# Kernel tuning notes

Hardware: AMD Instinct MI355X
Metric: run time of the kernel (lower is better)

## Reference

```python
import jax, jax.numpy as jnp
import numpy as np
from jax import lax

HIDDEN = 256
WIDTH = 1024
DEPTH = 4
T = 64
SUBSTEPS = 8  # fixed RK4 substeps per save interval (replaces diffrax adaptive Tsit5)

Y0 = np.array([0.0008417, 0.01495894, 0.00082556, 0.00068982, 0.00063456,
               0.00832867, 0.00190631, 0.00155624, 0.00142264, 0.01858621,
               0.02000239, 0.01796071, 0.01670121, 0.22218046, 0.02531468,
               0.03337227, 0.6147068], dtype=np.float32)


def setup_inputs() -> dict:
    key = jax.random.key(0)
    ks = jax.random.split(key, 8)

    def lin(k, out, inp):
        kw, kb = jax.random.split(k)
        lim = 1.0 / np.sqrt(inp)
        W = jax.random.uniform(kw, (out, inp), jnp.float32, -lim, lim)
        b = jax.random.uniform(kb, (out,), jnp.float32, -lim, lim)
        return W, b

    W0, b0 = lin(ks[0], WIDTH, HIDDEN + 17)
    Whs, bhs = [], []
    for i in range(DEPTH - 1):
        w, b = lin(ks[1 + i], WIDTH, WIDTH)
        Whs.append(w)
        bhs.append(b)
    Wh = jnp.stack(Whs)   # [DEPTH-1, WIDTH, WIDTH]
    bh = jnp.stack(bhs)   # [DEPTH-1, WIDTH]
    Wl, bl = lin(ks[4], HIDDEN, WIDTH)
    beta_W, beta_b = lin(ks[5], 1, HIDDEN)
    hvec = 0.01 * jax.random.normal(ks[6], (HIDDEN,), jnp.float32)
    scale = jnp.array([0.1], jnp.float32)
    y0_log = jnp.log(jnp.asarray(Y0))
    ts = jnp.arange(T, dtype=jnp.float32) * 0.25  # save points (months)
    return dict(ts=ts, W0=W0, b0=b0, Wh=Wh, bh=bh, Wl=Wl, bl=bl,
                beta_W=beta_W, beta_b=beta_b, hvec=hvec, scale=scale,
                y0_log=y0_log)


def _forward(ts, W0, b0, Wh, bh, Wl, bl, beta_W, beta_b, hvec, scale, y0_log):
    xi, mu, sigma, nu, gamma = 13/12, 0.041/12, 91/12, 36/12, 1.8/12

    def mlp(x):  # softplus hidden activations, final tanh(0.01*x)
        z = jax.nn.softplus(W0 @ x + b0)
        def body(z, wb):
            w, b = wb
            return jax.nn.softplus(w @ z + b), None
        z, _ = lax.scan(body, z, (Wh, bh))
        return jnp.tanh(0.01 * (Wl @ z + bl))

    def rhs(y):  # y = concat(state[17], h[HIDDEN])
        state, h = y[:17], y[17:]
        bb1 = 8.0 * jax.nn.sigmoid(beta_W @ h + beta_b)[0] + 25.0
        bb2, bb3, bb4 = 0.5 * bb1, 0.35 * bb1, 0.25 * bb1
        M, S1, E1, E2, E3, E4, I1, I2, I3, I4, R1, R2, R3, R4, S2, S3, S4 = state
        I = I1 + I2 + I3 + I4
        R = R1 + R2 + R3 + R4
        dstate = jnp.stack([
            R * mu - (xi + mu) * M,
            mu * (1 - R) + xi * M - mu * S1 - bb1 * I * S1,
            bb1 * I * S1 - (mu + sigma) * E1,
            bb2 * I * S2 - (mu + sigma) * E2,
            bb3 * I * S3 - (mu + sigma) * E3,
            bb4 * I * S4 - (mu + sigma) * E4,
            sigma * E1 - (nu + mu) * I1,
            sigma * E2 - (nu + mu) * I2,
            sigma * E3 - (nu + mu) * I3,
            sigma * E4 - (nu + mu) * I4,
            nu * I1 - (mu + gamma) * R1,
            nu * I2 - (mu + gamma) * R2,
            nu * I3 - (mu + gamma) * R3,
            nu * I4 - (mu + gamma) * R4,
            gamma * R1 - mu * S2 - bb2 * I * S2,
            gamma * R2 - mu * S3 - bb3 * I * S3,
            gamma * (R3 + R4) - mu * S4 - bb4 * I * S4,
        ])
        dh = scale[0] * mlp(jnp.concatenate([h, state]))
        return jnp.concatenate([dstate, dh])

    def rk4(y, dt):
        k1 = rhs(y)
        k2 = rhs(y + 0.5 * dt * k1)
        k3 = rhs(y + 0.5 * dt * k2)
        k4 = rhs(y + dt * k3)
        return y + (dt / 6.0) * (k1 + 2 * k2 + 2 * k3 + k4)

    y0 = jnp.concatenate([jax.nn.softmax(y0_log), hvec])

    def interval(y, dt_i):
        dt = dt_i / SUBSTEPS
        def step(y, _):
            return rk4(y, dt), None
        y, _ = lax.scan(step, y, None, length=SUBSTEPS)
        return y, y

    dts = ts[1:] - ts[:-1]
    _, ys = lax.scan(interval, y0, dts)
    ys = jnp.concatenate([y0[None], ys], axis=0)  # [T, 17+HIDDEN]
    return ys[:, :17], ys[:, 17:]


def reference(ts, W0, b0, Wh, bh, Wl, bl, beta_W, beta_b, hvec, scale, y0_log):
    return _forward(ts, W0, b0, Wh, bh, Wl, bl, beta_W, beta_b, hvec, scale, y0_log)
```

## Files before the change

### kernel.cpp

```cpp
#include <hip/hip_runtime.h>
#include <math.h>

#define NBLK    32
#define NLAUNCH 256
#define BS      512
#define NSTATE  17
#define NH      256
#define NX      273
#define WID     1024
#define NT      64
#define NSUB    8
#define SLC     32
#define POLL_CAP 2000000

#define SCALE_P 32768.0f
#define INV_P   3.0517578125e-5f
#define BIAS_P  (1LL << 22)
#define BIAS32  (32LL << 22)
#define SCALE_D 1048576.0f
#define INV_D   9.5367431640625e-7f

typedef unsigned long long u64;
typedef unsigned int u32;

__device__ __forceinline__ float softplus_f(float v) {
    return fmaxf(v, 0.f) + log1pf(expf(-fabsf(v)));
}

__device__ __forceinline__ void acc_pack(u64* p, float p0, float p1) {
    long long q0 = llrintf(p0 * SCALE_P) + BIAS_P;
    long long q1 = llrintf(p1 * SCALE_P) + BIAS_P;
    u64 w = 1ULL + ((u64)q0 << 8) + ((u64)q1 << 36);
    asm volatile("global_atomic_add_x2 %0, %1, off" :: "v"(p), "v"(w) : "memory");
}
__device__ __forceinline__ void acc_dh(u64* p, float v) {
    long long q = llrintf(v * SCALE_D);
    u64 w = ((u64)q << 16) + 1ULL;
    asm volatile("global_atomic_add_x2 %0, %1, off" :: "v"(p), "v"(w) : "memory");
}
__device__ __forceinline__ u64 rmw_read(const u64* p) {
    u64 w;
    asm volatile("global_atomic_add_x2 %0, %1, %2, off sc0\n\t"
                 "s_waitcnt vmcnt(0)"
                 : "=&v"(w) : "v"(p), "v"(0ULL) : "memory");
    return w;
}
__device__ __forceinline__ void reset_async(u64* p) {
    asm volatile("global_atomic_swap_x2 %0, %1, off" :: "v"(p), "v"(0ULL) : "memory");
}

extern "C" __global__ __launch_bounds__(BS, 1) void ode_kernel(
    const float* __restrict__ ts,   const float* __restrict__ W0,
    const float* __restrict__ b0,   const float* __restrict__ Wh,
    const float* __restrict__ bh,   const float* __restrict__ Wl,
    const float* __restrict__ bl,   const float* __restrict__ betaW,
    const float* __restrict__ betab,const float* __restrict__ hvec,
    const float* __restrict__ scale,const float* __restrict__ y0log,
    float* __restrict__ out, u64* hacc1, u64* hacc2, u64* hacc3,
    u64* dhacc, unsigned* ctrl)
{
    const int t = threadIdx.x;

    __shared__ int role_sh;
    __shared__ __align__(16) float y_s[NX];
    __shared__ __align__(16) float yn_s[NX];
    __shared__ __align__(16) float xm[NX];
    __shared__ __align__(16) float k_s[NX];
    __shared__ __align__(16) float z1_s[SLC];
    __shared__ __align__(16) float h1_s[SLC];
    __shared__ __align__(16) float h2_s[SLC];
    __shared__ __align__(16) float h3_s[SLC];
    __shared__ float red[8];
    __shared__ float dt_sh;
    extern __shared__ float wh3c[];

    if (t == 0) {
        int xcd;
        asm volatile("s_getreg_b32 %0, hwreg(HW_REG_XCC_ID)" : "=s"(xcd));
        xcd &= 7;
        unsigned rk = atomicAdd(&ctrl[xcd], 1u);
        if (rk == NBLK - 1) atomicCAS(&ctrl[8], 0u, (unsigned)(xcd + 1));
        unsigned w; int it = 0;
        do {
            w = __hip_atomic_load(&ctrl[8], __ATOMIC_RELAXED, __HIP_MEMORY_SCOPE_AGENT);
        } while (w == 0u && ++it < POLL_CAP);
        role_sh = (w != 0u && xcd == (int)w - 1 && rk < NBLK) ? (int)rk : -1;
    }
    __syncthreads();
    const int blk = role_sh;
    if (blk < 0) return;

    const float scale0 = scale[0];
    const float betab0 = betab[0];

    const int rowH = t >> 4, laneH = t & 15;
    const int growH = blk * SLC + rowH;
    const int r0 = 2 * t, r1 = 2 * t + 1;

    const float b0r    = b0[growH];
    const float betaWr = (t < NH) ? betaW[t] : 0.f;
    const float blr    = (t < NH) ? bl[t] : 0.f;
    float bhc[3];
    float bhc_o[3];
    if (t < 16) {
        bhc[0]   = bh[blk * SLC + 2 * t];
        bhc_o[0] = bh[blk * SLC + 2 * t + 1];
        bhc[1]   = bh[WID + blk * SLC + 2 * t];
        bhc_o[1] = bh[WID + blk * SLC + 2 * t + 1];
        bhc[2]   = bh[2 * WID + blk * SLC + 2 * t];
        bhc_o[2] = bh[2 * WID + blk * SLC + 2 * t + 1];
    }

    float w0r[18];
    {
        const float* w0p = W0 + (size_t)growH * NX;
        #pragma unroll
        for (int i = 0; i < 18; i++) {
            int c = laneH + i * 16;
            w0r[i] = (c < NX) ? w0p[c] : 0.f;
        }
    }
    float4 wc1a[8], wc1b[8], wc2a[8], wc2b[8];
    {
        const float* base0 = Wh + (size_t)r0 * WID + blk * SLC;
        const float* base1 = Wh + (size_t)r1 * WID + blk * SLC;
        #pragma unroll
        for (int q = 0; q < 8; q++) {
            wc1a[q] = *(const float4*)(base0 + q * 4);
            wc1b[q] = *(const float4*)(base1 + q * 4);
            wc2a[q] = *(const float4*)(base0 + (size_t)WID * WID + q * 4);
            wc2b[q] = *(const float4*)(base1 + (size_t)WID * WID + q * 4);
        }
    }
    {
        const float* src = Wh + 2 * (size_t)WID * WID;
        for (int i = t; i < WID * 8; i += BS) {
            int r = i >> 3, q = i & 7;
            float4 v = *(const float4*)(src + (size_t)r * WID + blk * SLC + q * 4);
            wh3c[(q * 4 + 0) * WID + r] = v.x;
            wh3c[(q * 4 + 1) * WID + r] = v.y;
            wh3c[(q * 4 + 2) * WID + r] = v.z;
            wh3c[(q * 4 + 3) * WID + r] = v.w;
        }
    }

    if (t < NSTATE) {
        float m = -1e30f;
        for (int j = 0; j < NSTATE; j++) m = fmaxf(m, y0log[j]);
        float ssum = 0.f;
        for (int j = 0; j < NSTATE; j++) ssum += expf(y0log[j] - m);
        y_s[t] = expf(y0log[t] - m) / ssum;
    }
    if (t < NH) y_s[NSTATE + t] = hvec[t];
    __syncthreads();

    if (blk == 0) {
        if (t < NSTATE) out[t] = y_s[t];
        if (t < NH)     out[NT * NSTATE + t] = y_s[NSTATE + t];
    }

    const float c_xi = 13.f / 12.f, c_mu = 0.041f / 12.f, c_sig = 91.f / 12.f,
                c_nu = 36.f / 12.f, c_gam = 1.8f / 12.f;

    long long prev_dh = 0;
    unsigned sidx = 0;

    for (int iv = 0; iv < NT - 1; iv++) {
        if (t == 0) dt_sh = (ts[iv + 1] - ts[iv]) * (1.f / NSUB);
        __syncthreads();
        const float dt = dt_sh;

        for (int sub = 0; sub < NSUB; sub++) {
            if (t < NX) yn_s[t] = y_s[t];

            for (int s = 0; s < 4; s++) {
                const float a   = (s == 0) ? 0.f : ((s == 3) ? 1.f : 0.5f);
                const float wgt = ((s == 0) || (s == 3)) ? dt * (1.f / 6.f) : dt * (1.f / 3.f);
                const float adt = a * dt;
                ++sidx;
                const int par = (int)(sidx & 1u);
                u64* h1p = hacc1 + par * 512;
                u64* h2p = hacc2 + par * 512;
                u64* h3p = hacc3 + par * 512;

                if (t < NX) {
                    const int src = (t < NH) ? (NSTATE + t) : (t - NH);
                    float v = y_s[src];
                    if (s != 0) v = fmaf(adt, k_s[src], v);
                    xm[t] = v;
                }
                __syncthreads();

                {
                    float acc = 0.f;
                    #pragma unroll
                    for (int i = 0; i < 18; i++) {
                        int c = laneH + i * 16;
                        if (c < NX) acc = fmaf(w0r[i], xm[c], acc);
                    }
                    #pragma unroll
                    for (int m = 1; m < 16; m <<= 1) acc += __shfl_xor(acc, m, 16);
                    if (laneH == 0) z1_s[rowH] = softplus_f(acc + b0r);
                }
                if (t < NH) {
                    float p = betaWr * xm[t];
                    #pragma unroll
                    for (int m = 1; m < 64; m <<= 1) p += __shfl_xor(p, m, 64);
                    if ((t & 63) == 0) red[t >> 6] = p;
                }
                __syncthreads();

                {
                    float p0 = 0.f, p1 = 0.f;
                    #pragma unroll
                    for (int q = 0; q < 8; q++) {
                        float4 z = *(const float4*)(z1_s + q * 4);
                        p0 = fmaf(wc1a[q].x, z.x, p0); p0 = fmaf(wc1a[q].y, z.y, p0);
                        p0 = fmaf(wc1a[q].z, z.z, p0); p0 = fmaf(wc1a[q].w, z.w, p0);
                        p1 = fmaf(wc1b[q].x, z.x, p1); p1 = fmaf(wc1b[q].y, z.y, p1);
                        p1 = fmaf(wc1b[q].z, z.z, p1); p1 = fmaf(wc1b[q].w, z.w, p1);
                    }
                    acc_pack(h1p + t, p0, p1);
                }

                if (t == 256) {
                    const float* xs = xm + NH;
                    float sd  = red[0] + red[1] + red[2] + red[3] + betab0;
                    float bb1 = 8.f / (1.f + expf(-sd)) + 25.f;
                    float bb2 = 0.5f * bb1, bb3 = 0.35f * bb1, bb4 = 0.25f * bb1;
                    float M  = xs[0],  S1 = xs[1],  E1 = xs[2],  E2 = xs[3];
                    float E3 = xs[4],  E4 = xs[5],  I1 = xs[6],  I2 = xs[7];
                    float I3 = xs[8],  I4 = xs[9],  R1 = xs[10], R2 = xs[11];
                    float R3 = xs[12], R4 = xs[13], S2 = xs[14], S3 = xs[15];
                    float S4 = xs[16];
                    float I = I1 + I2 + I3 + I4, Rs = R1 + R2 + R3 + R4;
                    k_s[0]  = Rs * c_mu - (c_xi + c_mu) * M;
                    k_s[1]  = c_mu * (1.f - Rs) + c_xi * M - c_mu * S1 - bb1 * I * S1;
                    k_s[2]  = bb1 * I * S1 - (c_mu + c_sig) * E1;
                    k_s[3]  = bb2 * I * S2 - (c_mu + c_sig) * E2;
                    k_s[4]  = bb3 * I * S3 - (c_mu + c_sig) * E3;
                    k_s[5]  = bb4 * I * S4 - (c_mu + c_sig) * E4;
                    k_s[6]  = c_sig * E1 - (c_nu + c_mu) * I1;
                    k_s[7]  = c_sig * E2 - (c_nu + c_mu) * I2;
                    k_s[8]  = c_sig * E3 - (c_nu + c_mu) * I3;
                    k_s[9]  = c_sig * E4 - (c_nu + c_mu) * I4;
                    k_s[10] = c_nu * I1 - (c_mu + c_gam) * R1;
                    k_s[11] = c_nu * I2 - (c_mu + c_gam) * R2;
                    k_s[12] = c_nu * I3 - (c_mu + c_gam) * R3;
                    k_s[13] = c_nu * I4 - (c_mu + c_gam) * R4;
                    k_s[14] = c_gam * R1 - c_mu * S2 - bb2 * I * S2;
                    k_s[15] = c_gam * R2 - c_mu * S3 - bb3 * I * S3;
                    k_s[16] = c_gam * (R3 + R4) - c_mu * S4 - bb4 * I * S4;
                }

                if (t < 16) {
                    u64* p = h1p + blk * 16 + t;
                    u64 w; int it = 0;
                    do { w = rmw_read(p); } while ((w & 0xFFu) != 32u && ++it < POLL_CAP);
                    reset_async(p);
                    long long v0 = (long long)((w >> 8) & 0xFFFFFFFULL) - BIAS32;
                    long long v1 = (long long)(w >> 36) - BIAS32;
                    h1_s[2 * t]     = softplus_f((float)v0 * INV_P + bhc[0]);
                    h1_s[2 * t + 1] = softplus_f((float)v1 * INV_P + bhc_o[0]);
                }
                __syncthreads();

                {
                    float p0 = 0.f, p1 = 0.f;
                    #pragma unroll
                    for (int q = 0; q < 8; q++) {
                        float4 z = *(const float4*)(h1_s + q * 4);
                        p0 = fmaf(wc2a[q].x, z.x, p0); p0 = fmaf(wc2a[q].y, z.y, p0);
                        p0 = fmaf(wc2a[q].z, z.z, p0); p0 = fmaf(wc2a[q].w, z.w, p0);
                        p1 = fmaf(wc2b[q].x, z.x, p1); p1 = fmaf(wc2b[q].y, z.y, p1);
                        p1 = fmaf(wc2b[q].z, z.z, p1); p1 = fmaf(wc2b[q].w, z.w, p1);
                    }
                    acc_pack(h2p + t, p0, p1);
                }
                if (t < 16) {
                    u64* p = h2p + blk * 16 + t;
                    u64 w; int it = 0;
                    do { w = rmw_read(p); } while ((w & 0xFFu) != 32u && ++it < POLL_CAP);
                    reset_async(p);
                    long long v0 = (long long)((w >> 8) & 0xFFFFFFFULL) - BIAS32;
                    long long v1 = (long long)(w >> 36) - BIAS32;
                    h2_s[2 * t]     = softplus_f((float)v0 * INV_P + bhc[1]);
                    h2_s[2 * t + 1] = softplus_f((float)v1 * INV_P + bhc_o[1]);
                }
                __syncthreads();

                {
                    float p0 = 0.f, p1 = 0.f;
                    #pragma unroll
                    for (int j = 0; j < SLC; j++) {
                        float hv = h2_s[j];
                        float2 wv = *(const float2*)(wh3c + j * WID + r0);
                        p0 = fmaf(wv.x, hv, p0);
                        p1 = fmaf(wv.y, hv, p1);
                    }
                    acc_pack(h3p + t, p0, p1);
                }
                float4 wvL[8];
                if (t < NH) {
                    const float* wp = Wl + (size_t)t * WID + blk * SLC;
                    #pragma unroll
                    for (int q = 0; q < 8; q++) wvL[q] = *(const float4*)(wp + q * 4);
                }
                if (t < 16) {
                    u64* p = h3p + blk * 16 + t;
                    u64 w; int it = 0;
                    do { w = rmw_read(p); } while ((w & 0xFFu) != 32u && ++it < POLL_CAP);
                    reset_async(p);
                    long long v0 = (long long)((w >> 8) & 0xFFFFFFFULL) - BIAS32;
                    long long v1 = (long long)(w >> 36) - BIAS32;
                    h3_s[2 * t]     = softplus_f((float)v0 * INV_P + bhc[2]);
                    h3_s[2 * t + 1] = softplus_f((float)v1 * INV_P + bhc_o[2]);
                }
                __syncthreads();

                if (t < NH) {
                    float p = 0.f;
                    #pragma unroll
                    for (int q = 0; q < 8; q++) {
                        float4 z = *(const float4*)(h3_s + q * 4);
                        p = fmaf(wvL[q].x, z.x, p); p = fmaf(wvL[q].y, z.y, p);
                        p = fmaf(wvL[q].z, z.z, p); p = fmaf(wvL[q].w, z.w, p);
                    }
                    acc_dh(dhacc + t, p);

                    u64* dp = dhacc + t;
                    const u32 tgt = (32u * sidx) & 0xFFFFu;
                    u64 w; int it = 0;
                    do { w = rmw_read(dp); } while ((u32)(w & 0xFFFFu) != tgt && ++it < POLL_CAP);
                    long long val = ((long long)w) >> 16;
                    long long diff = val - prev_dh;
                    prev_dh = val;
                    float accv = (float)diff * INV_D;
                    k_s[NSTATE + t] = scale0 * tanhf(0.01f * (accv + blr));
                }
                __syncthreads();
                if (t < NX) yn_s[t] = fmaf(wgt, k_s[t], yn_s[t]);
            }

            __syncthreads();
            if (t < NX) y_s[t] = yn_s[t];
            __syncthreads();
        }

        if (blk == 0) {
            if (t < NSTATE) out[(iv + 1) * NSTATE + t] = y_s[t];
            if (t < NH)     out[NT * NSTATE + (iv + 1) * NH + t] = y_s[NSTATE + t];
        }
    }
}

extern "C" void kernel_launch(void* const* d_in, const int* in_sizes, int n_in,
                              void* d_out, int out_size, void* d_ws, size_t ws_size,
                              hipStream_t stream) {
    const float* ts    = (const float*)d_in[0];
    const float* W0    = (const float*)d_in[1];
    const float* b0    = (const float*)d_in[2];
    const float* Wh    = (const float*)d_in[3];
    const float* bh    = (const float*)d_in[4];
    const float* Wl    = (const float*)d_in[5];
    const float* bl    = (const float*)d_in[6];
    const float* betaW = (const float*)d_in[7];
    const float* betab = (const float*)d_in[8];
    const float* hvec  = (const float*)d_in[9];
    const float* scale = (const float*)d_in[10];
    const float* y0log = (const float*)d_in[11];
    float* out = (float*)d_out;

    u64*      hacc1 = (u64*)d_ws;
    u64*      hacc2 = (u64*)((char*)d_ws + 8192);
    u64*      hacc3 = (u64*)((char*)d_ws + 16384);
    u64*      dhacc = (u64*)((char*)d_ws + 24576);
    unsigned* ctrl  = (unsigned*)((char*)d_ws + 26624);

    static int lds_set = 0;
    if (!lds_set) {
        hipFuncSetAttribute((const void*)ode_kernel,
                            hipFuncAttributeMaxDynamicSharedMemorySize, 131072);
        lds_set = 1;
    }

    hipMemsetAsync(d_ws, 0, 26624 + 64, stream);
    hipLaunchKernelGGL(ode_kernel, dim3(NLAUNCH), dim3(BS), 131072, stream,
                       ts, W0, b0, Wh, bh, Wl, bl, betaW, betab, hvec, scale,
                       y0log, out, hacc1, hacc2, hacc3, dhacc, ctrl);
}
```

Before: 21.15 ms.

## Pack final-layer dh accumulation into paired atomics with parity buffers and sleep polling

The final Wl layer now has each of 128 threads compute two output rows and push both in one packed 64-bit atomic. This replaces the per-row running-sum dh accumulator with parity double-buffered counters that are reset asynchronously during the next stage, halving the atomic traffic and the number of polling threads on the final reduction. All spin waits move into a helper that inserts s_sleep between polls to reduce contention on the atomic lines. Risks are lower dh precision (SCALE_P instead of SCALE_D), added polling latency from the sleep, and reliance on the reset of the other parity buffer being ordered correctly.

```diff
diff --git a/kernel.cpp b/kernel.cpp
--- a/kernel.cpp
+++ b/kernel.cpp
@@ -11,14 +11,12 @@
 #define NT      64
 #define NSUB    8
 #define SLC     32
-#define POLL_CAP 2000000
+#define POLL_CAP 500000
 
 #define SCALE_P 32768.0f
 #define INV_P   3.0517578125e-5f
 #define BIAS_P  (1LL << 22)
 #define BIAS32  (32LL << 22)
-#define SCALE_D 1048576.0f
-#define INV_D   9.5367431640625e-7f
 
 typedef unsigned long long u64;
 typedef unsigned int u32;
@@ -31,11 +29,6 @@
     long long q0 = llrintf(p0 * SCALE_P) + BIAS_P;
     long long q1 = llrintf(p1 * SCALE_P) + BIAS_P;
     u64 w = 1ULL + ((u64)q0 << 8) + ((u64)q1 << 36);
-    asm volatile("global_atomic_add_x2 %0, %1, off" :: "v"(p), "v"(w) : "memory");
-}
-__device__ __forceinline__ void acc_dh(u64* p, float v) {
-    long long q = llrintf(v * SCALE_D);
-    u64 w = ((u64)q << 16) + 1ULL;
     asm volatile("global_atomic_add_x2 %0, %1, off" :: "v"(p), "v"(w) : "memory");
 }
 __device__ __forceinline__ u64 rmw_read(const u64* p) {
@@ -47,6 +40,15 @@
 }
 __device__ __forceinline__ void reset_async(u64* p) {
     asm volatile("global_atomic_swap_x2 %0, %1, off" :: "v"(p), "v"(0ULL) : "memory");
+}
+__device__ __forceinline__ u64 poll32(const u64* p) {
+    u64 w; int it = 0;
+    for (;;) {
+        w = rmw_read(p);
+        if ((w & 0xFFu) == 32u || ++it > POLL_CAP) break;
+        asm volatile("s_sleep 1");
+    }
+    return w;
 }
 
 extern "C" __global__ __launch_bounds__(BS, 1) void ode_kernel(
@@ -83,7 +85,7 @@
         unsigned w; int it = 0;
         do {
             w = __hip_atomic_load(&ctrl[8], __ATOMIC_RELAXED, __HIP_MEMORY_SCOPE_AGENT);
-        } while (w == 0u && ++it < POLL_CAP);
+        } while (w == 0u && ++it < 2000000);
         role_sh = (w != 0u && xcd == (int)w - 1 && rk < NBLK) ? (int)rk : -1;
     }
     __syncthreads();
@@ -99,9 +101,9 @@
 
     const float b0r    = b0[growH];
     const float betaWr = (t < NH) ? betaW[t] : 0.f;
-    const float blr    = (t < NH) ? bl[t] : 0.f;
-    float bhc[3];
-    float bhc_o[3];
+    float bl0 = 0.f, bl1 = 0.f;
+    if (t < 128) { bl0 = bl[2 * t]; bl1 = bl[2 * t + 1]; }
+    float bhc[3], bhc_o[3];
     if (t < 16) {
         bhc[0]   = bh[blk * SLC + 2 * t];
         bhc_o[0] = bh[blk * SLC + 2 * t + 1];
@@ -162,7 +164,6 @@
     const float c_xi = 13.f / 12.f, c_mu = 0.041f / 12.f, c_sig = 91.f / 12.f,
                 c_nu = 36.f / 12.f, c_gam = 1.8f / 12.f;
 
-    long long prev_dh = 0;
     unsigned sidx = 0;
 
     for (int iv = 0; iv < NT - 1; iv++) {
@@ -182,6 +183,8 @@
                 u64* h1p = hacc1 + par * 512;
                 u64* h2p = hacc2 + par * 512;
                 u64* h3p = hacc3 + par * 512;
+                u64* dhp = dhacc + par * 128;
+                u64* dhq = dhacc + (par ^ 1) * 128;
 
                 if (t < NX) {
                     const int src = (t < NH) ? (NSTATE + t) : (t - NH);
@@ -255,9 +258,9 @@
 
                 if (t < 16) {
                     u64* p = h1p + blk * 16 + t;
-                    u64 w; int it = 0;
-                    do { w = rmw_read(p); } while ((w & 0xFFu) != 32u && ++it < POLL_CAP);
+                    u64 w = poll32(p);
                     reset_async(p);
+                    if (t < 4) reset_async(dhq + blk * 4 + t);
                     long long v0 = (long long)((w >> 8) & 0xFFFFFFFULL) - BIAS32;
                     long long v1 = (long long)(w >> 36) - BIAS32;
                     h1_s[2 * t]     = softplus_f((float)v0 * INV_P + bhc[0]);
@@ -279,8 +282,7 @@
                 }
                 if (t < 16) {
                     u64* p = h2p + blk * 16 + t;
-                    u64 w; int it = 0;
-                    do { w = rmw_read(p); } while ((w & 0xFFu) != 32u && ++it < POLL_CAP);
+                    u64 w = poll32(p);
                     reset_async(p);
                     long long v0 = (long long)((w >> 8) & 0xFFFFFFFULL) - BIAS32;
                     long long v1 = (long long)(w >> 36) - BIAS32;
@@ -300,16 +302,19 @@
                     }
                     acc_pack(h3p + t, p0, p1);
                 }
-                float4 wvL[8];
-                if (t < NH) {
-                    const float* wp = Wl + (size_t)t * WID + blk * SLC;
-                    #pragma unroll
-                    for (int q = 0; q < 8; q++) wvL[q] = *(const float4*)(wp + q * 4);
+                float4 wvL0[8], wvL1[8];
+                if (t < 128) {
+                    const float* wp0 = Wl + (size_t)(2 * t) * WID + blk * SLC;
+                    const float* wp1 = Wl + (size_t)(2 * t + 1) * WID + blk * SLC;
+                    #pragma unroll
+                    for (int q = 0; q < 8; q++) {
+                        wvL0[q] = *(const float4*)(wp0 + q * 4);
+                        wvL1[q] = *(const float4*)(wp1 + q * 4);
+                    }
                 }
                 if (t < 16) {
                     u64* p = h3p + blk * 16 + t;
-                    u64 w; int it = 0;
-                    do { w = rmw_read(p); } while ((w & 0xFFu) != 32u && ++it < POLL_CAP);
+                    u64 w = poll32(p);
                     reset_async(p);
                     long long v0 = (long long)((w >> 8) & 0xFFFFFFFULL) - BIAS32;
                     long long v1 = (long long)(w >> 36) - BIAS32;
@@ -318,25 +323,24 @@
                 }
                 __syncthreads();
 
-                if (t < NH) {
-                    float p = 0.f;
+                if (t < 128) {
+                    float p0 = 0.f, p1 = 0.f;
                     #pragma unroll
                     for (int q = 0; q < 8; q++) {
                         float4 z = *(const float4*)(h3_s + q * 4);
-                        p = fmaf(wvL[q].x, z.x, p); p = fmaf(wvL[q].y, z.y, p);
-                        p = fmaf(wvL[q].z, z.z, p); p = fmaf(wvL[q].w, z.w, p);
-                    }
-                    acc_dh(dhacc + t, p);
-
-                    u64* dp = dhacc + t;
-                    const u32 tgt = (32u * sidx) & 0xFFFFu;
-                    u64 w; int it = 0;
-                    do { w = rmw_read(dp); } while ((u32)(w & 0xFFFFu) != tgt && ++it < POLL_CAP);
-                    long long val = ((long long)w) >> 16;
-                    long long diff = val - prev_dh;
-                    prev_dh = val;
-                    float accv = (float)diff * INV_D;
-                    k_s[NSTATE + t] = scale0 * tanhf(0.01f * (accv + blr));
+                        p0 = fmaf(wvL0[q].x, z.x, p0); p0 = fmaf(wvL0[q].y, z.y, p0);
+                        p0 = fmaf(wvL0[q].z, z.z, p0); p0 = fmaf(wvL0[q].w, z.w, p0);
+                        p1 = fmaf(wvL1[q].x, z.x, p1); p1 = fmaf(wvL1[q].y, z.y, p1);
+                        p1 = fmaf(wvL1[q].z, z.z, p1); p1 = fmaf(wvL1[q].w, z.w, p1);
+                    }
+                    acc_pack(dhp + t, p0, p1);
+
+                    u64 w = poll32(dhp + t);
+                    long long v0 = (long long)((w >> 8) & 0xFFFFFFFULL) - BIAS32;
+                    long long v1 = (long long)(w >> 36) - BIAS32;
+                    float a0 = (float)v0 * INV_P, a1 = (float)v1 * INV_P;
+                    k_s[NSTATE + 2 * t]     = scale0 * tanhf(0.01f * (a0 + bl0));
+                    k_s[NSTATE + 2 * t + 1] = scale0 * tanhf(0.01f * (a1 + bl1));
                 }
                 __syncthreads();
                 if (t < NX) yn_s[t] = fmaf(wgt, k_s[t], yn_s[t]);
```

Result: slower. 27.36 ms (+29.4%).

## Repartition MLP into 4x8 block tiling with groups of 8 per atomic accumulator

Applied to the files above, without the earlier changes.

Each of the 32 blocks now owns a 128-column slice and a 128-row chunk of the hidden layers instead of a 32-column slice. So each packed atomic accumulator waits on 8 contributors rather than 32, and accumulator resets move off the critical polling path. Weights are no longer kept resident in registers or LDS; they are reloaded from global memory (L2/cache) every substep. This trades fewer cross-block contributors per sync for repeated weight traffic and a serial 69-step W0 loop per thread.

```diff
diff --git a/kernel.cpp b/kernel.cpp
--- a/kernel.cpp
+++ b/kernel.cpp
@@ -10,13 +10,12 @@
 #define WID     1024
 #define NT      64
 #define NSUB    8
-#define SLC     32
-#define POLL_CAP 2000000
+#define POLL_CAP 500000
 
 #define SCALE_P 32768.0f
 #define INV_P   3.0517578125e-5f
 #define BIAS_P  (1LL << 22)
-#define BIAS32  (32LL << 22)
+#define BIAS8   (8LL << 22)
 #define SCALE_D 1048576.0f
 #define INV_D   9.5367431640625e-7f
 
@@ -47,6 +46,11 @@
 }
 __device__ __forceinline__ void reset_async(u64* p) {
     asm volatile("global_atomic_swap_x2 %0, %1, off" :: "v"(p), "v"(0ULL) : "memory");
+}
+__device__ __forceinline__ u64 poll_cnt8(const u64* p) {
+    u64 w; int it = 0;
+    do { w = rmw_read(p); } while ((w & 0xFFu) != 8u && ++it < POLL_CAP);
+    return w;
 }
 
 extern "C" __global__ __launch_bounds__(BS, 1) void ode_kernel(
@@ -66,13 +70,14 @@
     __shared__ __align__(16) float yn_s[NX];
     __shared__ __align__(16) float xm[NX];
     __shared__ __align__(16) float k_s[NX];
-    __shared__ __align__(16) float z1_s[SLC];
-    __shared__ __align__(16) float h1_s[SLC];
-    __shared__ __align__(16) float h2_s[SLC];
-    __shared__ __align__(16) float h3_s[SLC];
+    __shared__ __align__(16) float z1_s[128];
+    __shared__ __align__(16) float h1_s[128];
+    __shared__ __align__(16) float h2_s[128];
+    __shared__ __align__(16) float h3_s[128];
     __shared__ float red[8];
     __shared__ float dt_sh;
-    extern __shared__ float wh3c[];
+    extern __shared__ float lds_pad[];
+    (void)lds_pad;
 
     if (t == 0) {
         int xcd;
@@ -83,7 +88,7 @@
         unsigned w; int it = 0;
         do {
             w = __hip_atomic_load(&ctrl[8], __ATOMIC_RELAXED, __HIP_MEMORY_SCOPE_AGENT);
-        } while (w == 0u && ++it < POLL_CAP);
+        } while (w == 0u && ++it < 2000000);
         role_sh = (w != 0u && xcd == (int)w - 1 && rk < NBLK) ? (int)rk : -1;
     }
     __syncthreads();
@@ -93,56 +98,34 @@
     const float scale0 = scale[0];
     const float betab0 = betab[0];
 
-    const int rowH = t >> 4, laneH = t & 15;
-    const int growH = blk * SLC + rowH;
-    const int r0 = 2 * t, r1 = 2 * t + 1;
-
-    const float b0r    = b0[growH];
+    const int sb = blk >> 2;
+    const int qb = blk & 3;
+
+    const int zrl = t >> 2, zc4 = t & 3;
+    const float b0r = b0[128 * sb + zrl];
+    const float* w0p = W0 + (size_t)(128 * sb + zrl) * NX;
+
+    const int pw   = t >> 2;
+    const int widx = 128 * qb + pw;
+    const int r0g  = 2 * widx;
+    const int colg = 128 * sb + 32 * zc4;
+    const int coll = 32 * zc4;
+    const float* w1a = Wh + (size_t)r0g * WID + colg;
+    const float* w1b = Wh + (size_t)(r0g + 1) * WID + colg;
+    const float* w2a = w1a + (size_t)WID * WID;
+    const float* w2b = w1b + (size_t)WID * WID;
+    const float* w3a = w2a + (size_t)WID * WID;
+    const float* w3b = w2b + (size_t)WID * WID;
+
+    float be[3], bo[3];
+    if (t < 64) {
+        be[0] = bh[128 * sb + 2 * t];            bo[0] = bh[128 * sb + 2 * t + 1];
+        be[1] = bh[WID + 128 * sb + 2 * t];      bo[1] = bh[WID + 128 * sb + 2 * t + 1];
+        be[2] = bh[2 * WID + 128 * sb + 2 * t];  bo[2] = bh[2 * WID + 128 * sb + 2 * t + 1];
+    }
+    const float* wlp = Wl + (size_t)t * WID + 128 * sb + 32 * qb;
+    const float blr  = (t < NH) ? bl[t] : 0.f;
     const float betaWr = (t < NH) ? betaW[t] : 0.f;
-    const float blr    = (t < NH) ? bl[t] : 0.f;
-    float bhc[3];
-    float bhc_o[3];
-    if (t < 16) {
-        bhc[0]   = bh[blk * SLC + 2 * t];
-        bhc_o[0] = bh[blk * SLC + 2 * t + 1];
-        bhc[1]   = bh[WID + blk * SLC + 2 * t];
-        bhc_o[1] = bh[WID + blk * SLC + 2 * t + 1];
-        bhc[2]   = bh[2 * WID + blk * SLC + 2 * t];
-        bhc_o[2] = bh[2 * WID + blk * SLC + 2 * t + 1];
-    }
-
-    float w0r[18];
-    {
-        const float* w0p = W0 + (size_t)growH * NX;
-        #pragma unroll
-        for (int i = 0; i < 18; i++) {
-            int c = laneH + i * 16;
-            w0r[i] = (c < NX) ? w0p[c] : 0.f;
-        }
-    }
-    float4 wc1a[8], wc1b[8], wc2a[8], wc2b[8];
-    {
-        const float* base0 = Wh + (size_t)r0 * WID + blk * SLC;
-        const float* base1 = Wh + (size_t)r1 * WID + blk * SLC;
-        #pragma unroll
-        for (int q = 0; q < 8; q++) {
-            wc1a[q] = *(const float4*)(base0 + q * 4);
-            wc1b[q] = *(const float4*)(base1 + q * 4);
-            wc2a[q] = *(const float4*)(base0 + (size_t)WID * WID + q * 4);
-            wc2b[q] = *(const float4*)(base1 + (size_t)WID * WID + q * 4);
-        }
-    }
-    {
-        const float* src = Wh + 2 * (size_t)WID * WID;
-        for (int i = t; i < WID * 8; i += BS) {
-            int r = i >> 3, q = i & 7;
-            float4 v = *(const float4*)(src + (size_t)r * WID + blk * SLC + q * 4);
-            wh3c[(q * 4 + 0) * WID + r] = v.x;
-            wh3c[(q * 4 + 1) * WID + r] = v.y;
-            wh3c[(q * 4 + 2) * WID + r] = v.z;
-            wh3c[(q * 4 + 3) * WID + r] = v.w;
-        }
-    }
 
     if (t < NSTATE) {
         float m = -1e30f;
@@ -193,14 +176,13 @@
 
                 {
                     float acc = 0.f;
-                    #pragma unroll
-                    for (int i = 0; i < 18; i++) {
-                        int c = laneH + i * 16;
-                        if (c < NX) acc = fmaf(w0r[i], xm[c], acc);
-                    }
-                    #pragma unroll
-                    for (int m = 1; m < 16; m <<= 1) acc += __shfl_xor(acc, m, 16);
-                    if (laneH == 0) z1_s[rowH] = softplus_f(acc + b0r);
+                    for (int i = 0; i < 69; i++) {
+                        int c = zc4 + 4 * i;
+                        if (c < NX) acc = fmaf(w0p[c], xm[c], acc);
+                    }
+                    acc += __shfl_xor(acc, 1, 4);
+                    acc += __shfl_xor(acc, 2, 4);
+                    if (zc4 == 0) z1_s[zrl] = softplus_f(acc + b0r);
                 }
                 if (t < NH) {
                     float p = betaWr * xm[t];
@@ -214,13 +196,17 @@
                     float p0 = 0.f, p1 = 0.f;
                     #pragma unroll
                     for (int q = 0; q < 8; q++) {
-                        float4 z = *(const float4*)(z1_s + q * 4);
-                        p0 = fmaf(wc1a[q].x, z.x, p0); p0 = fmaf(wc1a[q].y, z.y, p0);
-                        p0 = fmaf(wc1a[q].z, z.z, p0); p0 = fmaf(wc1a[q].w, z.w, p0);
-                        p1 = fmaf(wc1b[q].x, z.x, p1); p1 = fmaf(wc1b[q].y, z.y, p1);
-                        p1 = fmaf(wc1b[q].z, z.z, p1); p1 = fmaf(wc1b[q].w, z.w, p1);
-                    }
-                    acc_pack(h1p + t, p0, p1);
+                        float4 wa = *(const float4*)(w1a + 4 * q);
+                        float4 wb = *(const float4*)(w1b + 4 * q);
+                        float4 z  = *(const float4*)(z1_s + coll + 4 * q);
+                        p0 = fmaf(wa.x, z.x, p0); p0 = fmaf(wa.y, z.y, p0);
+                        p0 = fmaf(wa.z, z.z, p0); p0 = fmaf(wa.w, z.w, p0);
+                        p1 = fmaf(wb.x, z.x, p1); p1 = fmaf(wb.y, z.y, p1);
+                        p1 = fmaf(wb.z, z.z, p1); p1 = fmaf(wb.w, z.w, p1);
+                    }
+                    p0 += __shfl_xor(p0, 1, 4); p0 += __shfl_xor(p0, 2, 4);
+                    p1 += __shfl_xor(p1, 1, 4); p1 += __shfl_xor(p1, 2, 4);
+                    if (zc4 == 0) acc_pack(h1p + widx, p0, p1);
                 }
 
                 if (t == 256) {
@@ -253,15 +239,12 @@
                     k_s[16] = c_gam * (R3 + R4) - c_mu * S4 - bb4 * I * S4;
                 }
 
-                if (t < 16) {
-                    u64* p = h1p + blk * 16 + t;
-                    u64 w; int it = 0;
-                    do { w = rmw_read(p); } while ((w & 0xFFu) != 32u && ++it < POLL_CAP);
-                    reset_async(p);
-                    long long v0 = (long long)((w >> 8) & 0xFFFFFFFULL) - BIAS32;
-                    long long v1 = (long long)(w >> 36) - BIAS32;
-                    h1_s[2 * t]     = softplus_f((float)v0 * INV_P + bhc[0]);
-                    h1_s[2 * t + 1] = softplus_f((float)v1 * INV_P + bhc_o[0]);
+                if (t < 64) {
+                    u64 w = poll_cnt8(h1p + 64 * sb + t);
+                    long long v0 = (long long)((w >> 8) & 0xFFFFFFFULL) - BIAS8;
+                    long long v1 = (long long)(w >> 36) - BIAS8;
+                    h1_s[2 * t]     = softplus_f((float)v0 * INV_P + be[0]);
+                    h1_s[2 * t + 1] = softplus_f((float)v1 * INV_P + bo[0]);
                 }
                 __syncthreads();
 
@@ -269,52 +252,49 @@
                     float p0 = 0.f, p1 = 0.f;
                     #pragma unroll
                     for (int q = 0; q < 8; q++) {
-                        float4 z = *(const float4*)(h1_s + q * 4);
-                        p0 = fmaf(wc2a[q].x, z.x, p0); p0 = fmaf(wc2a[q].y, z.y, p0);
-                        p0 = fmaf(wc2a[q].z, z.z, p0); p0 = fmaf(wc2a[q].w, z.w, p0);
-                        p1 = fmaf(wc2b[q].x, z.x, p1); p1 = fmaf(wc2b[q].y, z.y, p1);
-                        p1 = fmaf(wc2b[q].z, z.z, p1); p1 = fmaf(wc2b[q].w, z.w, p1);
-                    }
-                    acc_pack(h2p + t, p0, p1);
-                }
-                if (t < 16) {
-                    u64* p = h2p + blk * 16 + t;
-                    u64 w; int it = 0;
-                    do { w = rmw_read(p); } while ((w & 0xFFu) != 32u && ++it < POLL_CAP);
-                    reset_async(p);
-                    long long v0 = (long long)((w >> 8) & 0xFFFFFFFULL) - BIAS32;
-                    long long v1 = (long long)(w >> 36) - BIAS32;
-                    h2_s[2 * t]     = softplus_f((float)v0 * INV_P + bhc[1]);
-                    h2_s[2 * t + 1] = softplus_f((float)v1 * INV_P + bhc_o[1]);
+                        float4 wa = *(const float4*)(w2a + 4 * q);
+                        float4 wb = *(const float4*)(w2b + 4 * q);
+                        float4 z  = *(const float4*)(h1_s + coll + 4 * q);
+                        p0 = fmaf(wa.x, z.x, p0); p0 = fmaf(wa.y, z.y, p0);
+                        p0 = fmaf(wa.z, z.z, p0); p0 = fmaf(wa.w, z.w, p0);
+                        p1 = fmaf(wb.x, z.x, p1); p1 = fmaf(wb.y, z.y, p1);
+                        p1 = fmaf(wb.z, z.z, p1); p1 = fmaf(wb.w, z.w, p1);
+                    }
+                    p0 += __shfl_xor(p0, 1, 4); p0 += __shfl_xor(p0, 2, 4);
+                    p1 += __shfl_xor(p1, 1, 4); p1 += __shfl_xor(p1, 2, 4);
+                    if (zc4 == 0) acc_pack(h2p + widx, p0, p1);
+                }
+                if (t < 64) {
+                    u64 w = poll_cnt8(h2p + 64 * sb + t);
+                    long long v0 = (long long)((w >> 8) & 0xFFFFFFFULL) - BIAS8;
+                    long long v1 = (long long)(w >> 36) - BIAS8;
+                    h2_s[2 * t]     = softplus_f((float)v0 * INV_P + be[1]);
+                    h2_s[2 * t + 1] = softplus_f((float)v1 * INV_P + bo[1]);
                 }
                 __syncthreads();
 
                 {
                     float p0 = 0.f, p1 = 0.f;
                     #pragma unroll
-                    for (int j = 0; j < SLC; j++) {
-                        float hv = h2_s[j];
-                        float2 wv = *(const float2*)(wh3c + j * WID + r0);
-                        p0 = fmaf(wv.x, hv, p0);
-                        p1 = fmaf(wv.y, hv, p1);
-                    }
-                    acc_pack(h3p + t, p0, p1);
-                }
-                float4 wvL[8];
-                if (t < NH) {
-                    const float* wp = Wl + (size_t)t * WID + blk * SLC;
-                    #pragma unroll
-                    for (int q = 0; q < 8; q++) wvL[q] = *(const float4*)(wp + q * 4);
-                }
-                if (t < 16) {
-                    u64* p = h3p + blk * 16 + t;
-                    u64 w; int it = 0;
-                    do { w = rmw_read(p); } while ((w & 0xFFu) != 32u && ++it < POLL_CAP);
-                    reset_async(p);
-                    long long v0 = (long long)((w >> 8) & 0xFFFFFFFULL) - BIAS32;
-                    long long v1 = (long long)(w >> 36) - BIAS32;
-                    h3_s[2 * t]     = softplus_f((float)v0 * INV_P + bhc[2]);
-                    h3_s[2 * t + 1] = softplus_f((float)v1 * INV_P + bhc_o[2]);
+                    for (int q = 0; q < 8; q++) {
+                        float4 wa = *(const float4*)(w3a + 4 * q);
+                        float4 wb = *(const float4*)(w3b + 4 * q);
+                        float4 z  = *(const float4*)(h2_s + coll + 4 * q);
+                        p0 = fmaf(wa.x, z.x, p0); p0 = fmaf(wa.y, z.y, p0);
+                        p0 = fmaf(wa.z, z.z, p0); p0 = fmaf(wa.w, z.w, p0);
+                        p1 = fmaf(wb.x, z.x, p1); p1 = fmaf(wb.y, z.y, p1);
+                        p1 = fmaf(wb.z, z.z, p1); p1 = fmaf(wb.w, z.w, p1);
+                    }
+                    p0 += __shfl_xor(p0, 1, 4); p0 += __shfl_xor(p0, 2, 4);
+                    p1 += __shfl_xor(p1, 1, 4); p1 += __shfl_xor(p1, 2, 4);
+                    if (zc4 == 0) acc_pack(h3p + widx, p0, p1);
+                }
+                if (t < 64) {
+                    u64 w = poll_cnt8(h3p + 64 * sb + t);
+                    long long v0 = (long long)((w >> 8) & 0xFFFFFFFULL) - BIAS8;
+                    long long v1 = (long long)(w >> 36) - BIAS8;
+                    h3_s[2 * t]     = softplus_f((float)v0 * INV_P + be[2]);
+                    h3_s[2 * t + 1] = softplus_f((float)v1 * INV_P + bo[2]);
                 }
                 __syncthreads();
 
@@ -322,21 +302,27 @@
                     float p = 0.f;
                     #pragma unroll
                     for (int q = 0; q < 8; q++) {
-                        float4 z = *(const float4*)(h3_s + q * 4);
-                        p = fmaf(wvL[q].x, z.x, p); p = fmaf(wvL[q].y, z.y, p);
-                        p = fmaf(wvL[q].z, z.z, p); p = fmaf(wvL[q].w, z.w, p);
+                        float4 wv = *(const float4*)(wlp + 4 * q);
+                        float4 z  = *(const float4*)(h3_s + 32 * qb + 4 * q);
+                        p = fmaf(wv.x, z.x, p); p = fmaf(wv.y, z.y, p);
+                        p = fmaf(wv.z, z.z, p); p = fmaf(wv.w, z.w, p);
                     }
                     acc_dh(dhacc + t, p);
 
-                    u64* dp = dhacc + t;
                     const u32 tgt = (32u * sidx) & 0xFFFFu;
                     u64 w; int it = 0;
-                    do { w = rmw_read(dp); } while ((u32)(w & 0xFFFFu) != tgt && ++it < POLL_CAP);
+                    do { w = rmw_read(dhacc + t); }
+                    while ((u32)(w & 0xFFFFu) != tgt && ++it < POLL_CAP);
                     long long val = ((long long)w) >> 16;
                     long long diff = val - prev_dh;
                     prev_dh = val;
-                    float accv = (float)diff * INV_D;
-                    k_s[NSTATE + t] = scale0 * tanhf(0.01f * (accv + blr));
+                    k_s[NSTATE + t] = scale0 * tanhf(0.01f * ((float)diff * INV_D + blr));
+                }
+                if (t < 16) {
+                    const int rw = 64 * sb + 16 * qb + t;
+                    reset_async(h1p + rw);
+                    reset_async(h2p + rw);
+                    reset_async(h3p + rw);
                 }
                 __syncthreads();
                 if (t < NX) yn_s[t] = fmaf(wgt, k_s[t], yn_s[t]);
@@ -380,12 +366,12 @@
     static int lds_set = 0;
     if (!lds_set) {
         hipFuncSetAttribute((const void*)ode_kernel,
-                            hipFuncAttributeMaxDynamicSharedMemorySize, 131072);
+                            hipFuncAttributeMaxDynamicSharedMemorySize, 98304);
         lds_set = 1;
     }
 
     hipMemsetAsync(d_ws, 0, 26624 + 64, stream);
-    hipLaunchKernelGGL(ode_kernel, dim3(NLAUNCH), dim3(BS), 131072, stream,
+    hipLaunchKernelGGL(ode_kernel, dim3(NLAUNCH), dim3(BS), 98304, stream,
                        ts, W0, b0, Wh, bh, Wl, bl, betaW, betab, hvec, scale,
                        y0log, out, hacc1, hacc2, hacc3, dhacc, ctrl);
 }
```

Measured after the change: 63.81 ms. +201.7%, slower.
